# Optimization experiments

Measured on AMD Instinct MI355X. Metric: run time of the kernel, lower is better.

## Reference

```python
import jax, jax.numpy as jnp
import numpy as np

N = 100000
E = 1600000
IN_DIM, H1, H2, H3 = 128, 128, 64, 32


def gcn_conv(x, edge_index, W, b, n):
    # PyG GCNConv (default): add self-loops, symmetric norm D^-1/2 (A+I) D^-1/2,
    # out[dst] = sum_{src->dst} norm * (x @ W)[src] + b
    src, dst = edge_index[0], edge_index[1]
    loops = jnp.arange(n)
    src = jnp.concatenate([src, loops])
    dst = jnp.concatenate([dst, loops])
    deg = jax.ops.segment_sum(jnp.ones((src.shape[0],), dtype=x.dtype), dst, num_segments=n)
    dinv = jnp.where(deg > 0, jax.lax.rsqrt(deg), jnp.zeros((), dtype=x.dtype))
    norm = dinv[src] * dinv[dst]  # [E+N]
    h = x @ W                      # [N, out_dim] dense transform first (out_dim <= in_dim)
    msg = h[src] * norm[:, None]   # [E+N, out_dim] gather + scale
    out = jax.ops.segment_sum(msg, dst, num_segments=n)
    return out + b


def setup_inputs() -> dict:
    key = jax.random.key(0)
    ks = jax.random.split(key, 10)
    def glorot(k, shape):
        lim = np.sqrt(6.0 / (shape[0] + shape[1]))
        return jax.random.uniform(k, shape, jnp.float32, -lim, lim)
    return {
        "x": jax.random.normal(ks[0], (N, IN_DIM), jnp.float32),
        "edge_index": jax.random.randint(ks[1], (2, E), 0, N, jnp.int64),
        "W1": glorot(ks[2], (IN_DIM, H1)), "b1": jnp.zeros((H1,), jnp.float32),
        "W2": glorot(ks[3], (H1, H2)),     "b2": jnp.zeros((H2,), jnp.float32),
        "W3": glorot(ks[4], (H2, H3)),     "b3": jnp.zeros((H3,), jnp.float32),
        "Wl": glorot(ks[5], (H3, 1)),      "bl": jnp.zeros((1,), jnp.float32),
    }


def reference(x, edge_index, W1, b1, W2, b2, W3, b3, Wl, bl):
    n = x.shape[0]
    h = jax.nn.relu(gcn_conv(x, edge_index, W1, b1, n))   # dropout p=0.5 is identity in eval
    h = jax.nn.relu(gcn_conv(h, edge_index, W2, b2, n))
    h = jax.nn.relu(gcn_conv(h, edge_index, W3, b3, n))
    return jax.nn.sigmoid(h @ Wl + bl)                    # [N, 1]
```

## Files before the change

kernel.cpp:

```cpp
#include <hip/hip_runtime.h>
#include <hip/hip_fp16.h>
#include <math.h>


#define BSHIFT 8
#define BNODES (1 << BSHIFT)
#define SRCBITS 17
#define MAXB 512

union H8 { float4 f4; __half2 h2[4]; };

typedef _Float16 half8 __attribute__((ext_vector_type(8)));
typedef float floatx4 __attribute__((ext_vector_type(4)));


__global__ __launch_bounds__(256) void k_hist(const int* __restrict__ dst, int E,
                                              int* __restrict__ bucketcnt, int B) {
    __shared__ int h[MAXB];
    int tid = threadIdx.x;
    h[tid] = 0; h[tid + 256] = 0;
    __syncthreads();
    for (int i = blockIdx.x * 256 + tid; i < E; i += gridDim.x * 256)
        atomicAdd(&h[dst[i] >> BSHIFT], 1);
    __syncthreads();
    if (tid < B && h[tid] > 0) atomicAdd(&bucketcnt[tid], h[tid]);
    int t2 = tid + 256;
    if (t2 < B && h[t2] > 0) atomicAdd(&bucketcnt[t2], h[t2]);
}

__global__ __launch_bounds__(512) void k_bscan(const int* __restrict__ bucketcnt,
                                               int* __restrict__ bucketbase,
                                               int* __restrict__ bucketfill,
                                               int* __restrict__ row_ptr,
                                               int B, int n, int E) {
    __shared__ int s[MAXB];
    int tid = threadIdx.x;
    int v = (tid < B) ? bucketcnt[tid] : 0;
    s[tid] = v;
    __syncthreads();
    for (int off = 1; off < MAXB; off <<= 1) {
        int t = (tid >= off) ? s[tid - off] : 0;
        __syncthreads();
        s[tid] += t;
        __syncthreads();
    }
    int excl = s[tid] - v;
    if (tid < B) { bucketbase[tid] = excl; bucketfill[tid] = excl; }
    if (tid == 0) { bucketbase[B] = E; row_ptr[n] = E; }
}

__global__ __launch_bounds__(256) void k_bucket(const int* __restrict__ src,
                                                const int* __restrict__ dst, int E,
                                                int* __restrict__ bucketfill,
                                                unsigned int* __restrict__ edgebuf,
                                                int B) {
    __shared__ int h[MAXB];
    __shared__ int cursor[MAXB];
    int tid = threadIdx.x;
    int base = blockIdx.x * 4096;
    int end = min(base + 4096, E);
    h[tid] = 0; h[tid + 256] = 0;
    __syncthreads();
    for (int i = base + tid; i < end; i += 256)
        atomicAdd(&h[dst[i] >> BSHIFT], 1);
    __syncthreads();
    if (tid < B) cursor[tid] = (h[tid] > 0) ? atomicAdd(&bucketfill[tid], h[tid]) : 0;
    int t2 = tid + 256;
    if (t2 < B) cursor[t2] = (h[t2] > 0) ? atomicAdd(&bucketfill[t2], h[t2]) : 0;
    __syncthreads();
    for (int i = base + tid; i < end; i += 256) {
        int d = dst[i];
        int b = d >> BSHIFT;
        unsigned int pk = ((unsigned int)(d & (BNODES - 1)) << SRCBITS) | (unsigned int)src[i];
        int pos = atomicAdd(&cursor[b], 1);
        edgebuf[pos] = pk;
    }
}

__global__ __launch_bounds__(256) void k_build(const unsigned int* __restrict__ edgebuf,
                                               const int* __restrict__ bucketbase,
                                               int* __restrict__ row_ptr,
                                               float* __restrict__ dinv,
                                               int* __restrict__ col, int n) {
    __shared__ int cnt[BNODES];
    __shared__ int s[BNODES];
    int b = blockIdx.x;
    int tid = threadIdx.x;
    int node0 = b << BSHIFT;
    int ebase = bucketbase[b], eend = bucketbase[b + 1];
    cnt[tid] = 0;
    __syncthreads();
    for (int i = ebase + tid; i < eend; i += 256)
        atomicAdd(&cnt[edgebuf[i] >> SRCBITS], 1);
    __syncthreads();
    int c = cnt[tid];
    s[tid] = c;
    __syncthreads();
    for (int off = 1; off < 256; off <<= 1) {
        int t = (tid >= off) ? s[tid - off] : 0;
        __syncthreads();
        s[tid] += t;
        __syncthreads();
    }
    int p = ebase + s[tid] - c;
    int node = node0 + tid;
    if (node < n) { row_ptr[node] = p; dinv[node] = rsqrtf((float)(c + 1)); }
    cnt[tid] = p;
    __syncthreads();
    for (int i = ebase + tid; i < eend; i += 256) {
        unsigned int pk = edgebuf[i];
        int pos = atomicAdd(&cnt[pk >> SRCBITS], 1);
        col[pos] = (int)(pk & ((1u << SRCBITS) - 1));
    }
}

__global__ void k_packW3(const float* __restrict__ W1, const float* __restrict__ W2,
                         const float* __restrict__ W3, _Float16* __restrict__ P1,
                         _Float16* __restrict__ P2, _Float16* __restrict__ P3) {
    int e = blockIdx.x * 256 + threadIdx.x;
    const float* W; _Float16* P; int OUT, idx;
    if (e < 16384)      { W = W1; P = P1; OUT = 128; idx = e; }
    else if (e < 24576) { W = W2; P = P2; OUT = 64;  idx = e - 16384; }
    else if (e < 26624) { W = W3; P = P3; OUT = 32;  idx = e - 24576; }
    else return;
    int j = idx & 7;
    int lane = (idx >> 3) & 63;
    int rest = idx >> 9;
    int NT = OUT >> 4;
    int t = rest % NT;
    int ss = rest / NT;
    int k = ss * 32 + (lane >> 4) * 8 + j;
    int nn = t * 16 + (lane & 15);
    P[idx] = (_Float16)W[k * OUT + nn];
}

template <int IN, int OUT>
__global__ __launch_bounds__(256) void k_matmul_mfma(const float* __restrict__ x,
                                                     const _Float16* __restrict__ Wpk,
                                                     const float* __restrict__ dinv,
                                                     __half* __restrict__ out, int n) {
    constexpr int S = IN / 32;
    constexpr int NT = OUT / 16;
    constexpr int TPW = NT / 2;
    constexpr int LDH = IN + 8;
    __shared__ _Float16 xs[32 * LDH];

    int tid = threadIdx.x;
    int rowbase = blockIdx.x * 32;

    constexpr int TOT = 32 * IN / 8;
    const float4* x4 = (const float4*)x;
    for (int i = tid; i < TOT; i += 256) {
        int r = i / (IN / 8), kg = i % (IN / 8);
        int row = rowbase + r;
        float4 a = make_float4(0.f, 0.f, 0.f, 0.f), b = a;
        if (row < n) {
            a = x4[(size_t)row * (IN / 4) + kg * 2 + 0];
            b = x4[(size_t)row * (IN / 4) + kg * 2 + 1];
        }
        _Float16* p = &xs[r * LDH + kg * 8];
        p[0] = (_Float16)a.x; p[1] = (_Float16)a.y;
        p[2] = (_Float16)a.z; p[3] = (_Float16)a.w;
        p[4] = (_Float16)b.x; p[5] = (_Float16)b.y;
        p[6] = (_Float16)b.z; p[7] = (_Float16)b.w;
    }
    __syncthreads();

    int lane = tid & 63;
    int wave = tid >> 6;
    int m = lane & 15, quad = lane >> 4;
    int rg = wave >> 1;
    int th = wave & 1;

    floatx4 acc[TPW];
#pragma unroll
    for (int t = 0; t < TPW; ++t) acc[t] = (floatx4){0.f, 0.f, 0.f, 0.f};

    const half8* Wf = (const half8*)Wpk;
#pragma unroll
    for (int s = 0; s < S; ++s) {
        half8 a = *(const half8*)&xs[(rg * 16 + m) * LDH + s * 32 + quad * 8];
#pragma unroll
        for (int t = 0; t < TPW; ++t) {
            half8 b = Wf[(s * NT + th * TPW + t) * 64 + lane];
            acc[t] = __builtin_amdgcn_mfma_f32_16x16x32_f16(a, b, acc[t], 0, 0, 0);
        }
    }

    int rbase = rowbase + rg * 16 + quad * 4;
#pragma unroll
    for (int r = 0; r < 4; ++r) {
        int row = rbase + r;
        if (row < n) {
            float dsc = dinv[row];
#pragma unroll
            for (int t = 0; t < TPW; ++t)
                out[(size_t)row * OUT + (th * TPW + t) * 16 + m] = __float2half(acc[t][r] * dsc);
        }
    }
}

template <int F, int OUT>
__global__ __launch_bounds__(256) void k_agg_mm(const __half* __restrict__ hs,
                                                const float* __restrict__ dinv,
                                                const float* __restrict__ bias,
                                                const int* __restrict__ row_ptr,
                                                const int* __restrict__ col,
                                                const _Float16* __restrict__ Wpk,
                                                __half* __restrict__ out, int n) {
    constexpr int S = F / 32;
    constexpr int NT = OUT / 16;
    constexpr int TPW = NT / 2;
    constexpr int LDH = F + 8;
    constexpr int LPN = F / 8;
    __shared__ _Float16 zs[32 * LDH];

    int tid = threadIdx.x;
    int rowbase = blockIdx.x * 32;
    const float4* h4 = (const float4*)hs;

    for (int task = tid; task < 32 * LPN; task += 256) {
        int nl = task / LPN;
        int fg = task % LPN;
        int node = rowbase + nl;
        H8 o;
        if (node < n) {
            float acc[8];
            H8 u;
            u.f4 = h4[(size_t)node * LPN + fg];
#pragma unroll
            for (int q = 0; q < 4; ++q) {
                float2 f = __half22float2(u.h2[q]);
                acc[2 * q + 0] = f.x;
                acc[2 * q + 1] = f.y;
            }
            int beg = row_ptr[node], end = row_ptr[node + 1];
            int j = beg;
            for (; j + 3 < end; j += 4) {
                int s0 = col[j], s1 = col[j + 1], s2 = col[j + 2], s3 = col[j + 3];
                H8 u0, u1, u2, u3;
                u0.f4 = h4[(size_t)s0 * LPN + fg];
                u1.f4 = h4[(size_t)s1 * LPN + fg];
                u2.f4 = h4[(size_t)s2 * LPN + fg];
                u3.f4 = h4[(size_t)s3 * LPN + fg];
#pragma unroll
                for (int q = 0; q < 4; ++q) {
                    float2 f0 = __half22float2(u0.h2[q]);
                    float2 f1 = __half22float2(u1.h2[q]);
                    float2 f2 = __half22float2(u2.h2[q]);
                    float2 f3 = __half22float2(u3.h2[q]);
                    acc[2 * q + 0] += (f0.x + f1.x) + (f2.x + f3.x);
                    acc[2 * q + 1] += (f0.y + f1.y) + (f2.y + f3.y);
                }
            }
            for (; j < end; ++j) {
                H8 u2;
                u2.f4 = h4[(size_t)col[j] * LPN + fg];
#pragma unroll
                for (int q = 0; q < 4; ++q) {
                    float2 f = __half22float2(u2.h2[q]);
                    acc[2 * q + 0] += f.x;
                    acc[2 * q + 1] += f.y;
                }
            }
            float dsc = dinv[node];
#pragma unroll
            for (int q = 0; q < 4; ++q) {
                float v0 = fmaxf(fmaf(acc[2 * q + 0], dsc, bias[fg * 8 + 2 * q + 0]), 0.f);
                float v1 = fmaxf(fmaf(acc[2 * q + 1], dsc, bias[fg * 8 + 2 * q + 1]), 0.f);
                o.h2[q] = __floats2half2_rn(v0, v1);
            }
        } else {
            o.f4 = make_float4(0.f, 0.f, 0.f, 0.f);
        }
        *(float4*)&zs[nl * LDH + fg * 8] = o.f4;
    }
    __syncthreads();

    int lane = tid & 63;
    int wave = tid >> 6;
    int m = lane & 15, quad = lane >> 4;
    int rg = wave >> 1;
    int th = wave & 1;

    floatx4 acc[TPW];
#pragma unroll
    for (int t = 0; t < TPW; ++t) acc[t] = (floatx4){0.f, 0.f, 0.f, 0.f};

    const half8* Wf = (const half8*)Wpk;
#pragma unroll
    for (int s = 0; s < S; ++s) {
        half8 a = *(const half8*)&zs[(rg * 16 + m) * LDH + s * 32 + quad * 8];
#pragma unroll
        for (int t = 0; t < TPW; ++t) {
            half8 b = Wf[(s * NT + th * TPW + t) * 64 + lane];
            acc[t] = __builtin_amdgcn_mfma_f32_16x16x32_f16(a, b, acc[t], 0, 0, 0);
        }
    }

    int rbase = rowbase + rg * 16 + quad * 4;
#pragma unroll
    for (int r = 0; r < 4; ++r) {
        int row = rbase + r;
        if (row < n) {
            float dsc = dinv[row];
#pragma unroll
            for (int t = 0; t < TPW; ++t)
                out[(size_t)row * OUT + (th * TPW + t) * 16 + m] = __float2half(acc[t][r] * dsc);
        }
    }
}

__global__ __launch_bounds__(256) void k_agg_final(const __half* __restrict__ hs,
                                                   const float* __restrict__ dinv,
                                                   const float* __restrict__ bias,
                                                   const int* __restrict__ row_ptr,
                                                   const int* __restrict__ col,
                                                   const float* __restrict__ Wl,
                                                   const float* __restrict__ bl,
                                                   float* __restrict__ out, int n) {
    constexpr int LPN = 4;
    int t = blockIdx.x * 256 + threadIdx.x;
    int node = t / LPN;
    int fg = t % LPN;
    if (node >= n) return;

    const float4* h4 = (const float4*)hs;
    float acc[8];
    {
        H8 u;
        u.f4 = h4[(size_t)node * LPN + fg];
#pragma unroll
        for (int q = 0; q < 4; ++q) {
            float2 f = __half22float2(u.h2[q]);
            acc[2 * q + 0] = f.x;
            acc[2 * q + 1] = f.y;
        }
    }
    int beg = row_ptr[node], end = row_ptr[node + 1];
    int j = beg;
    for (; j + 3 < end; j += 4) {
        int s0 = col[j], s1 = col[j + 1], s2 = col[j + 2], s3 = col[j + 3];
        H8 u0, u1, u2, u3;
        u0.f4 = h4[(size_t)s0 * LPN + fg];
        u1.f4 = h4[(size_t)s1 * LPN + fg];
        u2.f4 = h4[(size_t)s2 * LPN + fg];
        u3.f4 = h4[(size_t)s3 * LPN + fg];
#pragma unroll
        for (int q = 0; q < 4; ++q) {
            float2 f0 = __half22float2(u0.h2[q]);
            float2 f1 = __half22float2(u1.h2[q]);
            float2 f2 = __half22float2(u2.h2[q]);
            float2 f3 = __half22float2(u3.h2[q]);
            acc[2 * q + 0] += (f0.x + f1.x) + (f2.x + f3.x);
            acc[2 * q + 1] += (f0.y + f1.y) + (f2.y + f3.y);
        }
    }
    for (; j < end; ++j) {
        H8 u;
        u.f4 = h4[(size_t)col[j] * LPN + fg];
#pragma unroll
        for (int q = 0; q < 4; ++q) {
            float2 f = __half22float2(u.h2[q]);
            acc[2 * q + 0] += f.x;
            acc[2 * q + 1] += f.y;
        }
    }
    float dsc = dinv[node];
    float partial = 0.f;
#pragma unroll
    for (int k = 0; k < 8; ++k) {
        float v = fmaxf(fmaf(acc[k], dsc, bias[fg * 8 + k]), 0.f);
        partial = fmaf(v, Wl[fg * 8 + k], partial);
    }
    partial += __shfl_xor(partial, 1);
    partial += __shfl_xor(partial, 2);
    if (fg == 0) out[node] = 1.f / (1.f + expf(-(partial + bl[0])));
}

extern "C" void kernel_launch(void* const* d_in, const int* in_sizes, int n_in,
                              void* d_out, int out_size, void* d_ws, size_t ws_size,
                              hipStream_t stream) {
    const float* x  = (const float*)d_in[0];
    const int*   ei = (const int*)d_in[1];
    const float* W1 = (const float*)d_in[2];
    const float* b1 = (const float*)d_in[3];
    const float* W2 = (const float*)d_in[4];
    const float* b2 = (const float*)d_in[5];
    const float* W3 = (const float*)d_in[6];
    const float* b3 = (const float*)d_in[7];
    const float* Wl = (const float*)d_in[8];
    const float* bl = (const float*)d_in[9];

    const int N = in_sizes[0] / 128;
    const int E = in_sizes[1] / 2;
    const int* src = ei;
    const int* dst = ei + E;
    const int B = (N + BNODES - 1) >> BSHIFT;

    char* ws = (char*)d_ws;
    size_t off = 0;
    auto take = [&](size_t bytes) -> char* {
        char* p = ws + off;
        off += (bytes + 255) & ~(size_t)255;
        return p;
    };
    int*          bucketcnt  = (int*)take(MAXB * 4);
    int*          bucketbase = (int*)take((MAXB + 1) * 4);
    int*          bucketfill = (int*)take(MAXB * 4);
    unsigned int* edgebuf    = (unsigned int*)take((size_t)E * 4);
    int*          row_ptr    = (int*)take((size_t)(N + 1) * 4);
    float*        dinv       = (float*)take((size_t)N * 4);
    int*          col        = (int*)take((size_t)E * 4);
    __half*       bufA       = (__half*)take((size_t)N * 128 * 2);
    __half*       bufB       = (__half*)take((size_t)N * 128 * 2);
    _Float16*     Wpk1       = (_Float16*)take(128 * 128 * 2);
    _Float16*     Wpk2       = (_Float16*)take(128 * 64 * 2);
    _Float16*     Wpk3       = (_Float16*)take(64 * 32 * 2);
    (void)ws_size;

    hipMemsetAsync(bucketcnt, 0, MAXB * 4, stream);

    int gM = (N + 31) / 32;

    k_hist<<<512, 256, 0, stream>>>(dst, E, bucketcnt, B);
    k_bscan<<<1, MAXB, 0, stream>>>(bucketcnt, bucketbase, bucketfill, row_ptr, B, N, E);
    k_bucket<<<(E + 4095) / 4096, 256, 0, stream>>>(src, dst, E, bucketfill, edgebuf, B);
    k_build<<<B, 256, 0, stream>>>(edgebuf, bucketbase, row_ptr, dinv, col, N);

    k_packW3<<<(26624 + 255) / 256, 256, 0, stream>>>(W1, W2, W3, Wpk1, Wpk2, Wpk3);

    k_matmul_mfma<128, 128><<<gM, 256, 0, stream>>>(x, Wpk1, dinv, bufA, N);

    k_agg_mm<128, 64><<<gM, 256, 0, stream>>>(bufA, dinv, b1, row_ptr, col, Wpk2, bufB, N);

    k_agg_mm<64, 32><<<gM, 256, 0, stream>>>(bufB, dinv, b2, row_ptr, col, Wpk3, bufA, N);

    k_agg_final<<<((size_t)N * 4 + 255) / 256, 256, 0, stream>>>(
        bufA, dinv, b3, row_ptr, col, Wl, bl, (float*)d_out, N);
}
```

Before: 288.1 us.

## Build CSR with global-atomic degree count and direct scatter; unroll gather by eight

Replaces the two-pass bucketed CSR construction (bucket histogram, bucket scan, bucket scatter into a packed edge buffer, per-bucket local sort) with a per-node global atomic degree count, a three-kernel multi-block prefix scan, and a direct atomic scatter of sources into col. This removes the intermediate edge buffer pass but relies on scattered global atomics and random writes. The neighbour order inside each row now depends on atomic timing, so results can vary between runs. The aggregation loops also gain an 8-wide unrolled gather to put more independent loads in flight, at the cost of extra registers.

```diff
diff --git a/kernel.cpp b/kernel.cpp
--- a/kernel.cpp
+++ b/kernel.cpp
@@ -3,10 +3,7 @@
 #include <math.h>
 
 
-#define BSHIFT 8
-#define BNODES (1 << BSHIFT)
-#define SRCBITS 17
-#define MAXB 512
+#define SCAN_CHUNK 4096
 
 union H8 { float4 f4; __half2 h2[4]; };
 
@@ -14,87 +11,35 @@
 typedef float floatx4 __attribute__((ext_vector_type(4)));
 
 
-__global__ __launch_bounds__(256) void k_hist(const int* __restrict__ dst, int E,
-                                              int* __restrict__ bucketcnt, int B) {
-    __shared__ int h[MAXB];
+__global__ __launch_bounds__(256) void k_deg(const int* __restrict__ dst, int E,
+                                             int* __restrict__ deg) {
+    for (int i = blockIdx.x * 256 + threadIdx.x; i < E; i += gridDim.x * 256)
+        atomicAdd(&deg[dst[i]], 1);
+}
+
+__global__ __launch_bounds__(256) void k_scan1(const int* __restrict__ deg,
+                                               int* __restrict__ rp,
+                                               int* __restrict__ bsum, int n) {
+    __shared__ int s[256];
     int tid = threadIdx.x;
-    h[tid] = 0; h[tid + 256] = 0;
-    __syncthreads();
-    for (int i = blockIdx.x * 256 + tid; i < E; i += gridDim.x * 256)
-        atomicAdd(&h[dst[i] >> BSHIFT], 1);
-    __syncthreads();
-    if (tid < B && h[tid] > 0) atomicAdd(&bucketcnt[tid], h[tid]);
-    int t2 = tid + 256;
-    if (t2 < B && h[t2] > 0) atomicAdd(&bucketcnt[t2], h[t2]);
-}
-
-__global__ __launch_bounds__(512) void k_bscan(const int* __restrict__ bucketcnt,
-                                               int* __restrict__ bucketbase,
-                                               int* __restrict__ bucketfill,
-                                               int* __restrict__ row_ptr,
-                                               int B, int n, int E) {
-    __shared__ int s[MAXB];
-    int tid = threadIdx.x;
-    int v = (tid < B) ? bucketcnt[tid] : 0;
-    s[tid] = v;
-    __syncthreads();
-    for (int off = 1; off < MAXB; off <<= 1) {
-        int t = (tid >= off) ? s[tid - off] : 0;
-        __syncthreads();
-        s[tid] += t;
-        __syncthreads();
-    }
-    int excl = s[tid] - v;
-    if (tid < B) { bucketbase[tid] = excl; bucketfill[tid] = excl; }
-    if (tid == 0) { bucketbase[B] = E; row_ptr[n] = E; }
-}
-
-__global__ __launch_bounds__(256) void k_bucket(const int* __restrict__ src,
-                                                const int* __restrict__ dst, int E,
-                                                int* __restrict__ bucketfill,
-                                                unsigned int* __restrict__ edgebuf,
-                                                int B) {
-    __shared__ int h[MAXB];
-    __shared__ int cursor[MAXB];
-    int tid = threadIdx.x;
-    int base = blockIdx.x * 4096;
-    int end = min(base + 4096, E);
-    h[tid] = 0; h[tid + 256] = 0;
-    __syncthreads();
-    for (int i = base + tid; i < end; i += 256)
-        atomicAdd(&h[dst[i] >> BSHIFT], 1);
-    __syncthreads();
-    if (tid < B) cursor[tid] = (h[tid] > 0) ? atomicAdd(&bucketfill[tid], h[tid]) : 0;
-    int t2 = tid + 256;
-    if (t2 < B) cursor[t2] = (h[t2] > 0) ? atomicAdd(&bucketfill[t2], h[t2]) : 0;
-    __syncthreads();
-    for (int i = base + tid; i < end; i += 256) {
-        int d = dst[i];
-        int b = d >> BSHIFT;
-        unsigned int pk = ((unsigned int)(d & (BNODES - 1)) << SRCBITS) | (unsigned int)src[i];
-        int pos = atomicAdd(&cursor[b], 1);
-        edgebuf[pos] = pk;
-    }
-}
-
-__global__ __launch_bounds__(256) void k_build(const unsigned int* __restrict__ edgebuf,
-                                               const int* __restrict__ bucketbase,
-                                               int* __restrict__ row_ptr,
-                                               float* __restrict__ dinv,
-                                               int* __restrict__ col, int n) {
-    __shared__ int cnt[BNODES];
-    __shared__ int s[BNODES];
-    int b = blockIdx.x;
-    int tid = threadIdx.x;
-    int node0 = b << BSHIFT;
-    int ebase = bucketbase[b], eend = bucketbase[b + 1];
-    cnt[tid] = 0;
-    __syncthreads();
-    for (int i = ebase + tid; i < eend; i += 256)
-        atomicAdd(&cnt[edgebuf[i] >> SRCBITS], 1);
-    __syncthreads();
-    int c = cnt[tid];
-    s[tid] = c;
+    int base = blockIdx.x * SCAN_CHUNK + tid * 16;
+    int v[16];
+    int tot = 0;
+    if (base + 15 < n) {
+        const int4* d4 = (const int4*)(deg + base);
+#pragma unroll
+        for (int q = 0; q < 4; ++q) {
+            int4 t = d4[q];
+            v[4 * q + 0] = t.x; v[4 * q + 1] = t.y;
+            v[4 * q + 2] = t.z; v[4 * q + 3] = t.w;
+        }
+    } else {
+#pragma unroll
+        for (int k = 0; k < 16; ++k) v[k] = (base + k < n) ? deg[base + k] : 0;
+    }
+#pragma unroll
+    for (int k = 0; k < 16; ++k) tot += v[k];
+    s[tid] = tot;
     __syncthreads();
     for (int off = 1; off < 256; off <<= 1) {
         int t = (tid >= off) ? s[tid - off] : 0;
@@ -102,15 +47,67 @@
         s[tid] += t;
         __syncthreads();
     }
-    int p = ebase + s[tid] - c;
-    int node = node0 + tid;
-    if (node < n) { row_ptr[node] = p; dinv[node] = rsqrtf((float)(c + 1)); }
-    cnt[tid] = p;
+    int run = s[tid] - tot;
+#pragma unroll
+    for (int k = 0; k < 16; ++k) {
+        if (base + k < n) rp[base + k] = run;
+        run += v[k];
+    }
+    if (tid == 255) bsum[blockIdx.x] = s[255];
+}
+
+__global__ void k_scan2(int* bsum, int nb) {
+    __shared__ int s[64];
+    int tid = threadIdx.x;
+    int v = (tid < nb) ? bsum[tid] : 0;
+    s[tid] = v;
     __syncthreads();
-    for (int i = ebase + tid; i < eend; i += 256) {
-        unsigned int pk = edgebuf[i];
-        int pos = atomicAdd(&cnt[pk >> SRCBITS], 1);
-        col[pos] = (int)(pk & ((1u << SRCBITS) - 1));
+    for (int off = 1; off < 64; off <<= 1) {
+        int t = (tid >= off) ? s[tid - off] : 0;
+        __syncthreads();
+        s[tid] += t;
+        __syncthreads();
+    }
+    if (tid < nb) bsum[tid] = s[tid] - v;
+}
+
+__global__ __launch_bounds__(256) void k_scan3(const int* __restrict__ deg,
+                                               int* __restrict__ rp,
+                                               const int* __restrict__ bsum,
+                                               int* __restrict__ fill,
+                                               float* __restrict__ dinv, int n, int E) {
+    int i4 = blockIdx.x * 256 + threadIdx.x;
+    int i = i4 * 4;
+    if (i4 == 0) rp[n] = E;
+    if (i >= n) return;
+    int add = bsum[i >> 12];
+    if (i + 3 < n) {
+        int4 r = ((int4*)rp)[i4];
+        int4 d = ((const int4*)deg)[i4];
+        r.x += add; r.y += add; r.z += add; r.w += add;
+        ((int4*)rp)[i4] = r;
+        ((int4*)fill)[i4] = r;
+        float4 dv = make_float4(rsqrtf((float)(d.x + 1)), rsqrtf((float)(d.y + 1)),
+                                rsqrtf((float)(d.z + 1)), rsqrtf((float)(d.w + 1)));
+        ((float4*)dinv)[i4] = dv;
+    } else {
+        for (int k = 0; k < 4 && i + k < n; ++k) {
+            int r = rp[i + k] + add;
+            rp[i + k] = r;
+            fill[i + k] = r;
+            dinv[i + k] = rsqrtf((float)(deg[i + k] + 1));
+        }
+    }
+}
+
+__global__ __launch_bounds__(256) void k_scatter(const int* __restrict__ src,
+                                                 const int* __restrict__ dst, int E,
+                                                 int* __restrict__ fill,
+                                                 int* __restrict__ col) {
+    for (int i = blockIdx.x * 256 + threadIdx.x; i < E; i += gridDim.x * 256) {
+        int d = dst[i];
+        int pos = atomicAdd(&fill[d], 1);
+        col[pos] = src[i];
     }
 }
 
@@ -236,6 +233,32 @@
             }
             int beg = row_ptr[node], end = row_ptr[node + 1];
             int j = beg;
+            for (; j + 7 < end; j += 8) {
+                int c0 = col[j + 0], c1 = col[j + 1], c2 = col[j + 2], c3 = col[j + 3];
+                int c4 = col[j + 4], c5 = col[j + 5], c6 = col[j + 6], c7 = col[j + 7];
+                H8 u0, u1, u2, u3, u4, u5, u6, u7;
+                u0.f4 = h4[(size_t)c0 * LPN + fg];
+                u1.f4 = h4[(size_t)c1 * LPN + fg];
+                u2.f4 = h4[(size_t)c2 * LPN + fg];
+                u3.f4 = h4[(size_t)c3 * LPN + fg];
+                u4.f4 = h4[(size_t)c4 * LPN + fg];
+                u5.f4 = h4[(size_t)c5 * LPN + fg];
+                u6.f4 = h4[(size_t)c6 * LPN + fg];
+                u7.f4 = h4[(size_t)c7 * LPN + fg];
+#pragma unroll
+                for (int q = 0; q < 4; ++q) {
+                    float2 f0 = __half22float2(u0.h2[q]);
+                    float2 f1 = __half22float2(u1.h2[q]);
+                    float2 f2 = __half22float2(u2.h2[q]);
+                    float2 f3 = __half22float2(u3.h2[q]);
+                    float2 f4 = __half22float2(u4.h2[q]);
+                    float2 f5 = __half22float2(u5.h2[q]);
+                    float2 f6 = __half22float2(u6.h2[q]);
+                    float2 f7 = __half22float2(u7.h2[q]);
+                    acc[2 * q + 0] += ((f0.x + f1.x) + (f2.x + f3.x)) + ((f4.x + f5.x) + (f6.x + f7.x));
+                    acc[2 * q + 1] += ((f0.y + f1.y) + (f2.y + f3.y)) + ((f4.y + f5.y) + (f6.y + f7.y));
+                }
+            }
             for (; j + 3 < end; j += 4) {
                 int s0 = col[j], s1 = col[j + 1], s2 = col[j + 2], s3 = col[j + 3];
                 H8 u0, u1, u2, u3;
@@ -339,6 +362,32 @@
     }
     int beg = row_ptr[node], end = row_ptr[node + 1];
     int j = beg;
+    for (; j + 7 < end; j += 8) {
+        int c0 = col[j + 0], c1 = col[j + 1], c2 = col[j + 2], c3 = col[j + 3];
+        int c4 = col[j + 4], c5 = col[j + 5], c6 = col[j + 6], c7 = col[j + 7];
+        H8 u0, u1, u2, u3, u4, u5, u6, u7;
+        u0.f4 = h4[(size_t)c0 * LPN + fg];
+        u1.f4 = h4[(size_t)c1 * LPN + fg];
+        u2.f4 = h4[(size_t)c2 * LPN + fg];
+        u3.f4 = h4[(size_t)c3 * LPN + fg];
+        u4.f4 = h4[(size_t)c4 * LPN + fg];
+        u5.f4 = h4[(size_t)c5 * LPN + fg];
+        u6.f4 = h4[(size_t)c6 * LPN + fg];
+        u7.f4 = h4[(size_t)c7 * LPN + fg];
+#pragma unroll
+        for (int q = 0; q < 4; ++q) {
+            float2 f0 = __half22float2(u0.h2[q]);
+            float2 f1 = __half22float2(u1.h2[q]);
+            float2 f2 = __half22float2(u2.h2[q]);
+            float2 f3 = __half22float2(u3.h2[q]);
+            float2 f4 = __half22float2(u4.h2[q]);
+            float2 f5 = __half22float2(u5.h2[q]);
+            float2 f6 = __half22float2(u6.h2[q]);
+            float2 f7 = __half22float2(u7.h2[q]);
+            acc[2 * q + 0] += ((f0.x + f1.x) + (f2.x + f3.x)) + ((f4.x + f5.x) + (f6.x + f7.x));
+            acc[2 * q + 1] += ((f0.y + f1.y) + (f2.y + f3.y)) + ((f4.y + f5.y) + (f6.y + f7.y));
+        }
+    }
     for (; j + 3 < end; j += 4) {
         int s0 = col[j], s1 = col[j + 1], s2 = col[j + 2], s3 = col[j + 3];
         H8 u0, u1, u2, u3;
@@ -396,7 +445,6 @@
     const int E = in_sizes[1] / 2;
     const int* src = ei;
     const int* dst = ei + E;
-    const int B = (N + BNODES - 1) >> BSHIFT;
 
     char* ws = (char*)d_ws;
     size_t off = 0;
@@ -405,28 +453,29 @@
         off += (bytes + 255) & ~(size_t)255;
         return p;
     };
-    int*          bucketcnt  = (int*)take(MAXB * 4);
-    int*          bucketbase = (int*)take((MAXB + 1) * 4);
-    int*          bucketfill = (int*)take(MAXB * 4);
-    unsigned int* edgebuf    = (unsigned int*)take((size_t)E * 4);
-    int*          row_ptr    = (int*)take((size_t)(N + 1) * 4);
-    float*        dinv       = (float*)take((size_t)N * 4);
-    int*          col        = (int*)take((size_t)E * 4);
-    __half*       bufA       = (__half*)take((size_t)N * 128 * 2);
-    __half*       bufB       = (__half*)take((size_t)N * 128 * 2);
-    _Float16*     Wpk1       = (_Float16*)take(128 * 128 * 2);
-    _Float16*     Wpk2       = (_Float16*)take(128 * 64 * 2);
-    _Float16*     Wpk3       = (_Float16*)take(64 * 32 * 2);
+    int*      deg     = (int*)take((size_t)N * 4);
+    int*      bsum    = (int*)take(64 * 4);
+    int*      row_ptr = (int*)take((size_t)(N + 1) * 4);
+    int*      fill    = (int*)take((size_t)N * 4);
+    float*    dinv    = (float*)take((size_t)N * 4);
+    int*      col     = (int*)take((size_t)E * 4);
+    __half*   bufA    = (__half*)take((size_t)N * 128 * 2);
+    __half*   bufB    = (__half*)take((size_t)N * 128 * 2);
+    _Float16* Wpk1    = (_Float16*)take(128 * 128 * 2);
+    _Float16* Wpk2    = (_Float16*)take(128 * 64 * 2);
+    _Float16* Wpk3    = (_Float16*)take(64 * 32 * 2);
     (void)ws_size;
 
-    hipMemsetAsync(bucketcnt, 0, MAXB * 4, stream);
+    hipMemsetAsync(deg, 0, (size_t)N * 4, stream);
 
     int gM = (N + 31) / 32;
-
-    k_hist<<<512, 256, 0, stream>>>(dst, E, bucketcnt, B);
-    k_bscan<<<1, MAXB, 0, stream>>>(bucketcnt, bucketbase, bucketfill, row_ptr, B, N, E);
-    k_bucket<<<(E + 4095) / 4096, 256, 0, stream>>>(src, dst, E, bucketfill, edgebuf, B);
-    k_build<<<B, 256, 0, stream>>>(edgebuf, bucketbase, row_ptr, dinv, col, N);
+    int NB = (N + SCAN_CHUNK - 1) / SCAN_CHUNK;
+
+    k_deg<<<1024, 256, 0, stream>>>(dst, E, deg);
+    k_scan1<<<NB, 256, 0, stream>>>(deg, row_ptr, bsum, N);
+    k_scan2<<<1, 64, 0, stream>>>(bsum, NB);
+    k_scan3<<<((N + 3) / 4 + 255) / 256, 256, 0, stream>>>(deg, row_ptr, bsum, fill, dinv, N, E);
+    k_scatter<<<1024, 256, 0, stream>>>(src, dst, E, fill, col);
 
     k_packW3<<<(26624 + 255) / 256, 256, 0, stream>>>(W1, W2, W3, Wpk1, Wpk2, Wpk3);
 
```

Measured after the change: 454.6 us. +57.8%, slower.

## Split layer-2 aggregation from matmul with XCC-aware feature-half tiling

Applied to the files above, without the earlier changes.

Replaces the fused aggregate+matmul for layer 2 with a standalone aggregation kernel followed by a half-precision MFMA matmul. The aggregation kernel splits the 128 features into two halves and assigns each half to blocks on a matching XCC parity via an atomic tile counter. Each XCC's L2 then only has to cache half of the gathered feature rows, which targets L2 hit rate on the random neighbor gathers. The cost is an extra kernel launch, an extra write and read of an N×128 fp16 intermediate, and a counter memset.

```diff
diff --git a/kernel.cpp b/kernel.cpp
--- a/kernel.cpp
+++ b/kernel.cpp
@@ -200,6 +200,145 @@
     }
 }
 
+template <int IN, int OUT>
+__global__ __launch_bounds__(256) void k_matmul_mfma_h(const __half* __restrict__ z,
+                                                       const _Float16* __restrict__ Wpk,
+                                                       const float* __restrict__ dinv,
+                                                       __half* __restrict__ out, int n) {
+    constexpr int S = IN / 32;
+    constexpr int NT = OUT / 16;
+    constexpr int TPW = NT / 2;
+    constexpr int LDH = IN + 8;
+    __shared__ _Float16 xs[32 * LDH];
+
+    int tid = threadIdx.x;
+    int rowbase = blockIdx.x * 32;
+
+    constexpr int TOT = 32 * IN / 8;
+    const float4* z4 = (const float4*)z;
+    for (int i = tid; i < TOT; i += 256) {
+        int r = i / (IN / 8), kg = i % (IN / 8);
+        int row = rowbase + r;
+        float4 v = make_float4(0.f, 0.f, 0.f, 0.f);
+        if (row < n) v = z4[(size_t)row * (IN / 8) + kg];
+        *(float4*)&xs[r * LDH + kg * 8] = v;
+    }
+    __syncthreads();
+
+    int lane = tid & 63;
+    int wave = tid >> 6;
+    int m = lane & 15, quad = lane >> 4;
+    int rg = wave >> 1;
+    int th = wave & 1;
+
+    floatx4 acc[TPW];
+#pragma unroll
+    for (int t = 0; t < TPW; ++t) acc[t] = (floatx4){0.f, 0.f, 0.f, 0.f};
+
+    const half8* Wf = (const half8*)Wpk;
+#pragma unroll
+    for (int s = 0; s < S; ++s) {
+        half8 a = *(const half8*)&xs[(rg * 16 + m) * LDH + s * 32 + quad * 8];
+#pragma unroll
+        for (int t = 0; t < TPW; ++t) {
+            half8 b = Wf[(s * NT + th * TPW + t) * 64 + lane];
+            acc[t] = __builtin_amdgcn_mfma_f32_16x16x32_f16(a, b, acc[t], 0, 0, 0);
+        }
+    }
+
+    int rbase = rowbase + rg * 16 + quad * 4;
+#pragma unroll
+    for (int r = 0; r < 4; ++r) {
+        int row = rbase + r;
+        if (row < n) {
+            float dsc = dinv[row];
+#pragma unroll
+            for (int t = 0; t < TPW; ++t)
+                out[(size_t)row * OUT + (th * TPW + t) * 16 + m] = __float2half(acc[t][r] * dsc);
+        }
+    }
+}
+
+__global__ __launch_bounds__(256) void k_aggh128(const __half* __restrict__ hs,
+                                                 const float* __restrict__ dinv,
+                                                 const float* __restrict__ bias,
+                                                 const int* __restrict__ row_ptr,
+                                                 const int* __restrict__ col,
+                                                 int* __restrict__ ctr, int ntiles,
+                                                 __half* __restrict__ z, int n) {
+    __shared__ int s_tile, s_half;
+    if (threadIdx.x == 0) {
+        unsigned xcc;
+        asm volatile("s_getreg_b32 %0, hwreg(HW_REG_XCC_ID)" : "=s"(xcc));
+        int half = (int)(xcc & 1u);
+        int t = atomicAdd(&ctr[half], 1);
+        if (t >= ntiles) { t = atomicAdd(&ctr[half ^ 1], 1); half ^= 1; }
+        s_tile = t; s_half = half;
+    }
+    __syncthreads();
+    int tile = s_tile;
+    int half = s_half;
+    if (tile >= ntiles) return;
+
+    int tid = threadIdx.x;
+    int nl = tid >> 3;
+    int fgl = tid & 7;
+    int fg = half * 8 + fgl;
+    int node = tile * 32 + nl;
+    if (node >= n) return;
+
+    const float4* h4 = (const float4*)hs;
+    float acc[8];
+    {
+        H8 u;
+        u.f4 = h4[(size_t)node * 16 + fg];
+#pragma unroll
+        for (int q = 0; q < 4; ++q) {
+            float2 f = __half22float2(u.h2[q]);
+            acc[2 * q + 0] = f.x;
+            acc[2 * q + 1] = f.y;
+        }
+    }
+    int beg = row_ptr[node], end = row_ptr[node + 1];
+    int j = beg;
+    for (; j + 3 < end; j += 4) {
+        int s0 = col[j], s1 = col[j + 1], s2 = col[j + 2], s3 = col[j + 3];
+        H8 u0, u1, u2, u3;
+        u0.f4 = h4[(size_t)s0 * 16 + fg];
+        u1.f4 = h4[(size_t)s1 * 16 + fg];
+        u2.f4 = h4[(size_t)s2 * 16 + fg];
+        u3.f4 = h4[(size_t)s3 * 16 + fg];
+#pragma unroll
+        for (int q = 0; q < 4; ++q) {
+            float2 f0 = __half22float2(u0.h2[q]);
+            float2 f1 = __half22float2(u1.h2[q]);
+            float2 f2 = __half22float2(u2.h2[q]);
+            float2 f3 = __half22float2(u3.h2[q]);
+            acc[2 * q + 0] += (f0.x + f1.x) + (f2.x + f3.x);
+            acc[2 * q + 1] += (f0.y + f1.y) + (f2.y + f3.y);
+        }
+    }
+    for (; j < end; ++j) {
+        H8 u;
+        u.f4 = h4[(size_t)col[j] * 16 + fg];
+#pragma unroll
+        for (int q = 0; q < 4; ++q) {
+            float2 f = __half22float2(u.h2[q]);
+            acc[2 * q + 0] += f.x;
+            acc[2 * q + 1] += f.y;
+        }
+    }
+    float dsc = dinv[node];
+    H8 o;
+#pragma unroll
+    for (int q = 0; q < 4; ++q) {
+        float v0 = fmaxf(fmaf(acc[2 * q + 0], dsc, bias[fg * 8 + 2 * q + 0]), 0.f);
+        float v1 = fmaxf(fmaf(acc[2 * q + 1], dsc, bias[fg * 8 + 2 * q + 1]), 0.f);
+        o.h2[q] = __floats2half2_rn(v0, v1);
+    }
+    ((float4*)z)[(size_t)node * 16 + fg] = o.f4;
+}
+
 template <int F, int OUT>
 __global__ __launch_bounds__(256) void k_agg_mm(const __half* __restrict__ hs,
                                                 const float* __restrict__ dinv,
@@ -408,6 +547,7 @@
     int*          bucketcnt  = (int*)take(MAXB * 4);
     int*          bucketbase = (int*)take((MAXB + 1) * 4);
     int*          bucketfill = (int*)take(MAXB * 4);
+    int*          ctr        = (int*)take(2 * 4);
     unsigned int* edgebuf    = (unsigned int*)take((size_t)E * 4);
     int*          row_ptr    = (int*)take((size_t)(N + 1) * 4);
     float*        dinv       = (float*)take((size_t)N * 4);
@@ -420,6 +560,7 @@
     (void)ws_size;
 
     hipMemsetAsync(bucketcnt, 0, MAXB * 4, stream);
+    hipMemsetAsync(ctr, 0, 2 * 4, stream);
 
     int gM = (N + 31) / 32;
 
@@ -432,10 +573,12 @@
 
     k_matmul_mfma<128, 128><<<gM, 256, 0, stream>>>(x, Wpk1, dinv, bufA, N);
 
-    k_agg_mm<128, 64><<<gM, 256, 0, stream>>>(bufA, dinv, b1, row_ptr, col, Wpk2, bufB, N);
-
-    k_agg_mm<64, 32><<<gM, 256, 0, stream>>>(bufB, dinv, b2, row_ptr, col, Wpk3, bufA, N);
+    k_aggh128<<<2 * gM, 256, 0, stream>>>(bufA, dinv, b1, row_ptr, col, ctr, gM, bufB, N);
+
+    k_matmul_mfma_h<128, 64><<<gM, 256, 0, stream>>>(bufB, Wpk2, dinv, bufA, N);
+
+    k_agg_mm<64, 32><<<gM, 256, 0, stream>>>(bufA, dinv, b2, row_ptr, col, Wpk3, bufB, N);
 
     k_agg_final<<<((size_t)N * 4 + 255) / 256, 256, 0, stream>>>(
-        bufA, dinv, b3, row_ptr, col, Wl, bl, (float*)d_out, N);
-}
+        bufB, dinv, b3, row_ptr, col, Wl, bl, (float*)d_out, N);
+}
```

Result: slower. 345.2 us (+19.8%).
